# Performance work log

Hardware: AMD Instinct MI355X
Metric: run time of the kernel (lower is better)

Reference implementation:

```python
import jax, jax.numpy as jnp
import numpy as np

B, N, M = 2, 2048, 128
H, D = 16, 64
IN_DIM, CTX_DIM = 1024, 768


def layernorm(x, g, b, eps=1e-5):
    mu = x.mean(-1, keepdims=True)
    var = ((x - mu) ** 2).mean(-1, keepdims=True)
    return (x - mu) * jax.lax.rsqrt(var + eps) * g + b


def setup_inputs() -> dict:
    key = jax.random.key(0)
    ks = jax.random.split(key, 8)
    w = lambda i, sh: jax.random.normal(ks[i], sh, jnp.float32) * 0.02
    return {
        "x": jax.random.normal(ks[0], (B, N, IN_DIM), jnp.float32),
        "c_emb": jax.random.normal(ks[1], (B, M, CTX_DIM), jnp.float32),
        "ln_g": jnp.ones((IN_DIM,), jnp.float32),
        "ln_b": jnp.zeros((IN_DIM,), jnp.float32),
        "ctx_ln_g": jnp.ones((CTX_DIM,), jnp.float32),
        "ctx_ln_b": jnp.zeros((CTX_DIM,), jnp.float32),
        "W_ctx": w(2, (CTX_DIM, 2 * D)),
        "b_ctx": jnp.zeros((2 * D,), jnp.float32),
        "W_q": w(3, (IN_DIM, H * D)),
        "W_kv": w(4, (IN_DIM, 2 * H * D)),
        "null_kv": jax.random.normal(ks[5], (2, D), jnp.float32),
        "W_out": w(6, (H * D, IN_DIM)),
        "out_ln_g": jnp.ones((IN_DIM,), jnp.float32),
        "out_ln_b": jnp.zeros((IN_DIM,), jnp.float32),
    }


def reference(x, c_emb, ln_g, ln_b, ctx_ln_g, ctx_ln_b, W_ctx, b_ctx,
              W_q, W_kv, null_kv, W_out, out_ln_g, out_ln_b):
    b, n, _ = x.shape
    xn = layernorm(x, ln_g, ln_b)
    q = (xn @ W_q).reshape(b, n, H, D)                      # [b,n,h,d]
    kv = (xn @ W_kv).reshape(b, n, 2, H, D)
    k, v = kv[:, :, 0], kv[:, :, 1]                         # [b,n,h,d]
    # context projected to a single shared-across-heads k and v
    ckv = layernorm(c_emb, ctx_ln_g, ctx_ln_b) @ W_ctx + b_ctx
    ck, cv = jnp.split(ckv, 2, axis=-1)                     # [b,m,d]
    nk = jnp.broadcast_to(null_kv[0], (b, 1, D))
    nv = jnp.broadcast_to(null_kv[1], (b, 1, D))
    k_ext = jnp.concatenate([nk, ck], axis=1)               # [b,m+1,d]
    v_ext = jnp.concatenate([nv, cv], axis=1)
    scale = D ** -0.5
    s_self = jnp.einsum('bnhd,bkhd->bhnk', q, k) * scale    # [b,h,n,n]
    s_ctx = jnp.einsum('bnhd,bkd->bhnk', q, k_ext) * scale  # [b,h,n,m+1]
    w = jax.nn.softmax(jnp.concatenate([s_self, s_ctx], axis=-1), axis=-1)
    w_self, w_ctx = w[..., :n], w[..., n:]
    out = (jnp.einsum('bhnk,bkhd->bnhd', w_self, v)
           + jnp.einsum('bhnk,bkd->bnhd', w_ctx, v_ext))    # [b,n,h,d]
    out = out.reshape(b, n, H * D) @ W_out                  # [b,n,input_dim]
    return layernorm(out, out_ln_g, out_ln_b)
```

## Files before the change

### kernel.cpp

```cpp
#include <hip/hip_runtime.h>
#include <cstdint>
#include <cstddef>

typedef __attribute__((ext_vector_type(8))) short bf16x8;
typedef __attribute__((ext_vector_type(4))) short bf16x4;
typedef __attribute__((ext_vector_type(4))) float f32x4;
typedef __attribute__((ext_vector_type(4))) unsigned int u32x4;
typedef __attribute__((ext_vector_type(2))) unsigned int u32x2;

__device__ inline unsigned short f2b(float f){
  unsigned int u = __float_as_uint(f);
  u += 0x7fffu + ((u >> 16) & 1u);
  return (unsigned short)(u >> 16);
}
__device__ inline unsigned int pk2(float a, float b){
  unsigned int ua = __float_as_uint(a) + 0x8000u;
  unsigned int ub = __float_as_uint(b) + 0x8000u;
  return __builtin_amdgcn_perm(ub, ua, 0x07060302u);
}
__device__ inline void gl2lds16(const void* g, void* l){
  __builtin_amdgcn_global_load_lds(
      (const __attribute__((address_space(1))) unsigned int*)g,
      (__attribute__((address_space(3))) unsigned int*)l, 16, 0, 0);
}

#define QSCALE 0.18033688011112042f

__global__ __launch_bounds__(256) void prologue_kernel(
    const float* __restrict__ Wq, const float* __restrict__ Wkv,
    const float* __restrict__ Wout,
    unsigned short* __restrict__ Wqkv_t, unsigned short* __restrict__ Wout_t,
    const float* __restrict__ X, const float* __restrict__ G,
    const float* __restrict__ Bb, unsigned short* __restrict__ xn,
    const float* __restrict__ Cemb, const float* __restrict__ cG,
    const float* __restrict__ cBb, const float* __restrict__ Wctx,
    const float* __restrict__ bctx, const float* __restrict__ nullkv,
    unsigned short* __restrict__ kext, unsigned short* __restrict__ vext_t)
{
  __shared__ __align__(16) char fsm[9216];
  int bid = blockIdx.x;
  int t = threadIdx.x;

  if (bid < 1024){
    short* tile = (short*)fsm;
    int cg0 = (bid & 63) * 64;
    int kt  = (bid >> 6) * 64;
    const float* src; int ld; int col0; unsigned short* dst; int drow0;
    if (cg0 < 1024)      { src = Wq;   ld = 1024; col0 = cg0;        dst = Wqkv_t; drow0 = cg0; }
    else if (cg0 < 3072) { src = Wkv;  ld = 2048; col0 = cg0 - 1024; dst = Wqkv_t; drow0 = cg0; }
    else                 { src = Wout; ld = 1024; col0 = cg0 - 3072; dst = Wout_t; drow0 = cg0 - 3072; }
    #pragma unroll
    for (int i = 0; i < 16; ++i){
      int lin = t + 256*i;
      int k = lin >> 6, c = lin & 63;
      tile[k*72 + c] = (short)f2b(src[(size_t)(kt + k)*ld + col0 + c]);
    }
    __syncthreads();
    #pragma unroll
    for (int i = 0; i < 16; ++i){
      int lin = t + 256*i;
      int c = lin >> 6, k = lin & 63;
      dst[(size_t)(drow0 + c)*1024 + kt + k] = (unsigned short)tile[k*72 + c];
    }
  } else if (bid < 5120){
    int row = bid - 1024;
    float* red = (float*)fsm;
    float4 x = ((const float4*)(X + (size_t)row*1024))[t];
    float s  = x.x + x.y + x.z + x.w;
    float s2 = x.x*x.x + x.y*x.y + x.z*x.z + x.w*x.w;
    #pragma unroll
    for (int o = 32; o > 0; o >>= 1){ s += __shfl_down(s, o); s2 += __shfl_down(s2, o); }
    int w = t >> 6;
    if ((t & 63) == 0){ red[w] = s; red[4 + w] = s2; }
    __syncthreads();
    float mu  = (red[0]+red[1]+red[2]+red[3]) * (1.0f/1024.0f);
    float var = (red[4]+red[5]+red[6]+red[7]) * (1.0f/1024.0f) - mu*mu;
    float rstd = rsqrtf(var + 1e-5f);
    float4 g = ((const float4*)G)[t];
    float4 b = ((const float4*)Bb)[t];
    ushort4 u;
    u.x = f2b((x.x-mu)*rstd*g.x + b.x);
    u.y = f2b((x.y-mu)*rstd*g.y + b.y);
    u.z = f2b((x.z-mu)*rstd*g.z + b.z);
    u.w = f2b((x.w-mu)*rstd*g.w + b.w);
    ((ushort4*)xn)[(size_t)row*256 + t] = u;
  } else {
    int row = bid - 5120;
    int b = row >> 7, m = row & 127;
    bool act = t < 128;
    float* red  = (float*)fsm;
    float* xns  = (float*)(fsm + 16);
    if (act && row < 128){
      int b2 = row >> 6, fr = row & 63;
      int frow = (fr == 0) ? 0 : (128 + fr);
      if (t < 64){
        kext[((size_t)b2*192 + frow)*64 + t] = (frow == 0) ? f2b(nullkv[t]) : (unsigned short)0;
      } else {
        int d = t - 64;
        vext_t[((size_t)b2*64 + d)*192 + frow] = (frow == 0) ? f2b(nullkv[64 + d]) : (unsigned short)0;
      }
    }
    const float* xr = Cemb + (size_t)row*768;
    float v[6]; float s = 0.f, s2 = 0.f;
    if (act){
      #pragma unroll
      for (int j = 0; j < 6; ++j){ float xv = xr[t + 128*j]; v[j] = xv; s += xv; s2 += xv*xv; }
      #pragma unroll
      for (int o = 32; o > 0; o >>= 1){ s += __shfl_down(s, o); s2 += __shfl_down(s2, o); }
      int w = t >> 6;
      if ((t & 63) == 0){ red[w] = s; red[2 + w] = s2; }
    }
    __syncthreads();
    if (act){
      float mu  = (red[0]+red[1]) * (1.0f/768.0f);
      float var = (red[2]+red[3]) * (1.0f/768.0f) - mu*mu;
      float rstd = rsqrtf(var + 1e-5f);
      #pragma unroll
      for (int j = 0; j < 6; ++j){ int c = t + 128*j; xns[c] = (v[j]-mu)*rstd*cG[c] + cBb[c]; }
    }
    __syncthreads();
    if (act){
      float acc = bctx[t];
      #pragma unroll 8
      for (int j = 0; j < 768; ++j) acc += xns[j] * Wctx[j*128 + t];
      unsigned short hv = f2b(acc);
      if (t < 64) kext[((size_t)b*192 + 1 + m)*64 + t] = hv;
      else        vext_t[((size_t)b*64 + (t - 64))*192 + 1 + m] = hv;
    }
  }
}

__global__ __launch_bounds__(256) void ln1024f_kernel(
    const float* __restrict__ X, const float* __restrict__ G,
    const float* __restrict__ Bb, float* __restrict__ out)
{
  int row = blockIdx.x, t = threadIdx.x;
  float4 x = ((const float4*)(X + (size_t)row*1024))[t];
  float s  = x.x + x.y + x.z + x.w;
  float s2 = x.x*x.x + x.y*x.y + x.z*x.z + x.w*x.w;
  #pragma unroll
  for (int o = 32; o > 0; o >>= 1){ s += __shfl_down(s, o); s2 += __shfl_down(s2, o); }
  __shared__ float red[8];
  int w = t >> 6;
  if ((t & 63) == 0){ red[w] = s; red[4 + w] = s2; }
  __syncthreads();
  float mu  = (red[0]+red[1]+red[2]+red[3]) * (1.0f/1024.0f);
  float var = (red[4]+red[5]+red[6]+red[7]) * (1.0f/1024.0f) - mu*mu;
  float rstd = rsqrtf(var + 1e-5f);
  float4 g = ((const float4*)G)[t];
  float4 b = ((const float4*)Bb)[t];
  float4 y;
  y.x = (x.x-mu)*rstd*g.x + b.x;
  y.y = (x.y-mu)*rstd*g.y + b.y;
  y.z = (x.z-mu)*rstd*g.z + b.z;
  y.w = (x.w-mu)*rstd*g.w + b.w;
  ((float4*)out)[(size_t)row*256 + t] = y;
}

#define GEMM_MAINLOOP(A_, Bt_, tM_, tN_)                                        \
  __shared__ __align__(16) short sA[128*64];                                    \
  __shared__ __align__(16) short sB[128*64];                                    \
  int t = threadIdx.x, w = t >> 6, lane = t & 63;                               \
  int wm = w & 1, wn = w >> 1, lm = lane & 15, q = lane >> 4;                   \
  int grow = lane >> 3;                                                         \
  int gchk = ((lane & 7) ^ grow) << 3;                                          \
  f32x4 acc[4][4] = {};                                                         \
  const unsigned short* Aw = A_ + (size_t)(tM_ + w*32 + grow)*1024 + gchk;      \
  const unsigned short* Bw = Bt_ + (size_t)(tN_ + w*32 + grow)*1024 + gchk;     \
  for (int kk = 0; kk < 1024; kk += 64){                                        \
    __syncthreads();                                                            \
    gl2lds16(Aw + kk,            &sA[(w*32     )*64]);                          \
    gl2lds16(Aw + kk +  8*1024,  &sA[(w*32 +  8)*64]);                          \
    gl2lds16(Aw + kk + 16*1024,  &sA[(w*32 + 16)*64]);                          \
    gl2lds16(Aw + kk + 24*1024,  &sA[(w*32 + 24)*64]);                          \
    gl2lds16(Bw + kk,            &sB[(w*32     )*64]);                          \
    gl2lds16(Bw + kk +  8*1024,  &sB[(w*32 +  8)*64]);                          \
    gl2lds16(Bw + kk + 16*1024,  &sB[(w*32 + 16)*64]);                          \
    gl2lds16(Bw + kk + 24*1024,  &sB[(w*32 + 24)*64]);                          \
    __syncthreads();                                                            \
    bf16x8 af[4][2], bfr[4][2];                                                 \
    _Pragma("unroll")                                                           \
    for (int i = 0; i < 4; ++i){                                                \
      int ra = wm*64 + i*16 + lm, rb = wn*64 + i*16 + lm;                       \
      _Pragma("unroll")                                                         \
      for (int hh = 0; hh < 2; ++hh){                                           \
        int sw = ((hh*4 + q) ^ (lm & 7)) << 3;                                  \
        af[i][hh]  = *(const bf16x8*)(&sA[ra*64 + sw]);                         \
        bfr[i][hh] = *(const bf16x8*)(&sB[rb*64 + sw]);                         \
      }                                                                         \
    }                                                                           \
    _Pragma("unroll")                                                           \
    for (int hh = 0; hh < 2; ++hh)                                              \
      _Pragma("unroll")                                                         \
      for (int i = 0; i < 4; ++i)                                               \
        _Pragma("unroll")                                                       \
        for (int j = 0; j < 4; ++j)                                             \
          acc[i][j] = __builtin_amdgcn_mfma_f32_16x16x32_bf16(af[i][hh], bfr[j][hh], acc[i][j], 0, 0, 0); \
  }

__global__ __launch_bounds__(256) void gemm_qkv_kernel(
    const unsigned short* __restrict__ A, const unsigned short* __restrict__ Bt,
    unsigned short* __restrict__ Qb, unsigned short* __restrict__ Kb,
    unsigned short* __restrict__ VtG)
{
  int id = blockIdx.x;
  int xcd = id & 7, r = id >> 3;
  int tM = ((xcd >> 1)*8 + (r & 7)) * 128;
  int tN = ((xcd & 1)*12 + (r >> 3)) * 128;
  GEMM_MAINLOOP(A, Bt, tM, tN)
  if (tN < 1024){
    #pragma unroll
    for (int i = 0; i < 4; ++i){
      int R0 = tM + wm*64 + i*16 + q*4;
      int b = R0 >> 11, n = R0 & 2047;
      #pragma unroll
      for (int j = 0; j < 4; ++j){
        int Cg = tN + wn*64 + j*16 + lm;
        int h = Cg >> 6, d = Cg & 63;
        size_t base = ((((size_t)(b*16 + h) << 11) | n) << 6) + d;
        #pragma unroll
        for (int rr = 0; rr < 4; ++rr)
          Qb[base + (size_t)rr*64] = f2b(acc[i][j][rr] * QSCALE);
      }
    }
  } else if (tN < 2048){
    #pragma unroll
    for (int i = 0; i < 4; ++i){
      int R0 = tM + wm*64 + i*16 + q*4;
      int b = R0 >> 11, n = R0 & 2047;
      #pragma unroll
      for (int j = 0; j < 4; ++j){
        int c2 = tN - 1024 + wn*64 + j*16 + lm;
        int h = c2 >> 6, d = c2 & 63;
        size_t base = ((((size_t)(b*16 + h) << 11) | n) << 6) + d;
        #pragma unroll
        for (int rr = 0; rr < 4; ++rr)
          Kb[base + (size_t)rr*64] = f2b(acc[i][j][rr]);
      }
    }
  } else {
    #pragma unroll
    for (int i = 0; i < 4; ++i){
      int R0 = tM + wm*64 + i*16 + q*4;
      int b = R0 >> 11, n = R0 & 2047;
      #pragma unroll
      for (int j = 0; j < 4; ++j){
        int c2 = tN - 2048 + wn*64 + j*16 + lm;
        int h = c2 >> 6, d = c2 & 63;
        ushort4 u;
        u.x = f2b(acc[i][j][0]); u.y = f2b(acc[i][j][1]);
        u.z = f2b(acc[i][j][2]); u.w = f2b(acc[i][j][3]);
        *(ushort4*)(VtG + ((size_t)(b*16 + h)*64 + d)*2048 + n) = u;
      }
    }
  }
}

__global__ __launch_bounds__(256) void gemm_out_kernel(
    const unsigned short* __restrict__ A, const unsigned short* __restrict__ Bt,
    float* __restrict__ C)
{
  int id = blockIdx.x;
  int xcd = id & 7, r = id >> 3;
  int tM = ((r & 3)*8 + xcd) * 128;
  int tN = (r >> 2) * 128;
  GEMM_MAINLOOP(A, Bt, tM, tN)
  #pragma unroll
  for (int i = 0; i < 4; ++i){
    int R0 = tM + wm*64 + i*16 + q*4;
    #pragma unroll
    for (int j = 0; j < 4; ++j){
      int Cg = tN + wn*64 + j*16 + lm;
      #pragma unroll
      for (int rr = 0; rr < 4; ++rr)
        C[(size_t)(R0 + rr)*1024 + Cg] = acc[i][j][rr];
    }
  }
}

__global__ __launch_bounds__(256, 2) void attn_kernel(
    const unsigned short* __restrict__ Qb, const unsigned short* __restrict__ Kb,
    const unsigned short* __restrict__ VtG, const unsigned short* __restrict__ kext,
    const unsigned short* __restrict__ vext_t, unsigned short* __restrict__ Ob)
{
  __shared__ __align__(16) char smem[54272];
  int id = blockIdx.x;
  int xcd = id & 7, slot = id >> 3;
  int bh = xcd*4 + (slot >> 4);
  int qt = slot & 15;
  int b = bh >> 4, h = bh & 15;
  int t = threadIdx.x, w = t >> 6, lane = t & 63;
  int p = w >> 1, lw = w & 1;
  int lm = lane & 15, q = lane >> 4;

  short* myK = (short*)(smem + p*9216);
  short* myV = (short*)(smem + 18432 + p*9216);
  short* pw  = (short*)(smem + 36864 + w*4352);

  const unsigned short* Qbase = Qb + ((size_t)bh*2048 + qt*128 + lw*64)*64;
  bf16x8 qf[4][2];
  #pragma unroll
  for (int qq = 0; qq < 4; ++qq){
    qf[qq][0] = *(const bf16x8*)(Qbase + (size_t)(qq*16 + lm)*64 + q*8);
    qf[qq][1] = *(const bf16x8*)(Qbase + (size_t)(qq*16 + lm)*64 + q*8 + 32);
  }

  f32x4 o[4][4] = {};
  float l_i[4] = {0.f, 0.f, 0.f, 0.f};

  int pt = t & 127;
  int r0 = pt >> 1, c0 = (pt & 1) << 5;
  const int t0 = p ? 18 : 0;
  const int t1 = p ? 35 : 18;

  u32x4 kr[4], vr[4];
  {
    const unsigned short* kp = Kb + ((size_t)bh*2048 + t0*64 + r0)*64 + c0;
    const unsigned short* vp = VtG + ((size_t)bh*64 + r0)*2048 + t0*64 + c0;
    #pragma unroll
    for (int jj = 0; jj < 4; ++jj){
      kr[jj] = *(const u32x4*)(kp + 8*jj);
      vr[jj] = *(const u32x4*)(vp + 8*jj);
    }
  }

  for (int it = 0; it < 18; ++it){
    int tile = t0 + it;
    bool valid = tile < t1;
    __syncthreads();
    if (valid){
      #pragma unroll
      for (int jj = 0; jj < 4; ++jj){
        *(u32x4*)(&myK[r0*72 + c0 + 8*jj]) = kr[jj];
        *(u32x4*)(&myV[r0*72 + c0 + 8*jj]) = vr[jj];
      }
    }
    __syncthreads();

    int nt = tile + 1;
    if (nt < t1){
      bool ext = nt >= 32;
      int kb = ext ? (nt - 32)*64 : nt*64;
      const unsigned short* kp = ext ? (kext + ((size_t)b*192 + kb + r0)*64 + c0)
                                     : (Kb + ((size_t)bh*2048 + kb + r0)*64 + c0);
      const unsigned short* vp = ext ? (vext_t + ((size_t)b*64 + r0)*192 + kb + c0)
                                     : (VtG + ((size_t)bh*64 + r0)*2048 + kb + c0);
      #pragma unroll
      for (int jj = 0; jj < 4; ++jj){
        kr[jj] = *(const u32x4*)(kp + 8*jj);
        vr[jj] = *(const u32x4*)(vp + 8*jj);
      }
    }
    if (!valid) continue;

    bf16x8 kf[4][2];
    #pragma unroll
    for (int st = 0; st < 4; ++st){
      kf[st][0] = *(const bf16x8*)(&myK[(st*16 + lm)*72 + q*8]);
      kf[st][1] = *(const bf16x8*)(&myK[(st*16 + lm)*72 + q*8 + 32]);
    }

    #pragma unroll
    for (int qp = 0; qp < 2; ++qp){
      f32x4 s[2][4];
      #pragma unroll
      for (int qh = 0; qh < 2; ++qh){
        int qq = qp*2 + qh;
        #pragma unroll
        for (int st = 0; st < 4; ++st){
          f32x4 z = {};
          z = __builtin_amdgcn_mfma_f32_16x16x32_bf16(kf[st][0], qf[qq][0], z, 0, 0, 0);
          s[qh][st] = __builtin_amdgcn_mfma_f32_16x16x32_bf16(kf[st][1], qf[qq][1], z, 0, 0, 0);
        }
      }
      if (tile == 34){
        #pragma unroll
        for (int qh = 0; qh < 2; ++qh)
          #pragma unroll
          for (int st = 0; st < 4; ++st)
            #pragma unroll
            for (int rr = 0; rr < 4; ++rr){
              int key = 128 + st*16 + q*4 + rr;
              if (key >= 129) s[qh][st][rr] = -1e30f;
            }
      }
      #pragma unroll
      for (int qh = 0; qh < 2; ++qh){
        float sm = 0.f;
        #pragma unroll
        for (int st = 0; st < 4; ++st)
          #pragma unroll
          for (int rr = 0; rr < 4; ++rr){
            float pv = __builtin_amdgcn_exp2f(s[qh][st][rr]);
            s[qh][st][rr] = pv; sm += pv;
          }
        l_i[qp*2 + qh] += sm;
        #pragma unroll
        for (int st = 0; st < 4; ++st){
          u32x2 pkd;
          pkd[0] = pk2(s[qh][st][0], s[qh][st][1]);
          pkd[1] = pk2(s[qh][st][2], s[qh][st][3]);
          *(u32x2*)(&pw[(qh*16 + lm)*68 + st*16 + q*4]) = pkd;
        }
      }
      bf16x8 pb[2][2];
      #pragma unroll
      for (int qh = 0; qh < 2; ++qh){
        bf16x4 a0 = *(const bf16x4*)(&pw[(qh*16 + lm)*68 + q*8]);
        bf16x4 a1 = *(const bf16x4*)(&pw[(qh*16 + lm)*68 + q*8 + 4]);
        bf16x4 a2 = *(const bf16x4*)(&pw[(qh*16 + lm)*68 + 32 + q*8]);
        bf16x4 a3 = *(const bf16x4*)(&pw[(qh*16 + lm)*68 + 32 + q*8 + 4]);
        pb[qh][0] = __builtin_shufflevector(a0, a1, 0,1,2,3,4,5,6,7);
        pb[qh][1] = __builtin_shufflevector(a2, a3, 0,1,2,3,4,5,6,7);
      }
      #pragma unroll
      for (int ds = 0; ds < 4; ++ds){
        bf16x8 af0 = *(const bf16x8*)(&myV[(ds*16 + lm)*72 + q*8]);
        bf16x8 af1 = *(const bf16x8*)(&myV[(ds*16 + lm)*72 + q*8 + 32]);
        #pragma unroll
        for (int qh = 0; qh < 2; ++qh){
          int qq = qp*2 + qh;
          o[ds][qq] = __builtin_amdgcn_mfma_f32_16x16x32_bf16(af0, pb[qh][0], o[ds][qq], 0, 0, 0);
          o[ds][qq] = __builtin_amdgcn_mfma_f32_16x16x32_bf16(af1, pb[qh][1], o[ds][qq], 0, 0, 0);
        }
      }
    }
  }

  float* mb = (float*)smem;
  float* reg = mb + lw*4352 + lane*68;
  __syncthreads();
  if (p == 1){
    #pragma unroll
    for (int ds = 0; ds < 4; ++ds)
      #pragma unroll
      for (int qq = 0; qq < 4; ++qq)
        *(f32x4*)(reg + (ds*4 + qq)*4) = o[ds][qq];
    #pragma unroll
    for (int qq = 0; qq < 4; ++qq) reg[64 + qq] = l_i[qq];
  }
  __syncthreads();
  if (p == 0){
    #pragma unroll
    for (int qq = 0; qq < 4; ++qq){
      #pragma unroll
      for (int ds = 0; ds < 4; ++ds){
        f32x4 ov = *(const f32x4*)(reg + (ds*4 + qq)*4);
        o[ds][qq] += ov;
      }
      float l = l_i[qq] + reg[64 + qq];
      l += __shfl_xor(l, 16);
      l += __shfl_xor(l, 32);
      float inv = 1.0f / l;
      int n = qt*128 + lw*64 + qq*16 + lm;
      size_t base = ((size_t)b*2048 + n)*1024 + h*64 + q*4;
      #pragma unroll
      for (int ds = 0; ds < 4; ++ds){
        ushort4 u;
        u.x = f2b(o[ds][qq][0] * inv); u.y = f2b(o[ds][qq][1] * inv);
        u.z = f2b(o[ds][qq][2] * inv); u.w = f2b(o[ds][qq][3] * inv);
        *(ushort4*)(Ob + base + ds*16) = u;
      }
    }
  }
}

extern "C" void kernel_launch(void* const* d_in, const int* in_sizes, int n_in,
                              void* d_out, int out_size, void* d_ws, size_t ws_size,
                              hipStream_t stream)
{
  const float* x       = (const float*)d_in[0];
  const float* c_emb   = (const float*)d_in[1];
  const float* ln_g    = (const float*)d_in[2];
  const float* ln_b    = (const float*)d_in[3];
  const float* ctx_g   = (const float*)d_in[4];
  const float* ctx_b   = (const float*)d_in[5];
  const float* W_ctx   = (const float*)d_in[6];
  const float* b_ctx   = (const float*)d_in[7];
  const float* W_q     = (const float*)d_in[8];
  const float* W_kv    = (const float*)d_in[9];
  const float* null_kv = (const float*)d_in[10];
  const float* W_out   = (const float*)d_in[11];
  const float* oln_g   = (const float*)d_in[12];
  const float* oln_b   = (const float*)d_in[13];
  float* out = (float*)d_out;

  char* p = (char*)d_ws;
  unsigned short* xn     = (unsigned short*)p; p += (size_t)4096*1024*2;
  unsigned short* Wqkv_t = (unsigned short*)p; p += (size_t)3072*1024*2;
  unsigned short* Wout_t = (unsigned short*)p; p += (size_t)1024*1024*2;
  unsigned short* Qb     = (unsigned short*)p; p += (size_t)32*2048*64*2;
  unsigned short* Kb     = (unsigned short*)p; p += (size_t)32*2048*64*2;
  unsigned short* VtG    = (unsigned short*)p; p += (size_t)32*64*2048*2;
  unsigned short* kext   = (unsigned short*)p; p += (size_t)2*192*64*2;
  unsigned short* vext_t = (unsigned short*)p; p += (size_t)2*64*192*2;
  unsigned short* aout   = (unsigned short*)p; p += (size_t)4096*1024*2;
  float*          ptmp   = (float*)p;          p += (size_t)4096*1024*4;

  prologue_kernel<<<5376, 256, 0, stream>>>(
      W_q, W_kv, W_out, Wqkv_t, Wout_t,
      x, ln_g, ln_b, xn,
      c_emb, ctx_g, ctx_b, W_ctx, b_ctx, null_kv, kext, vext_t);
  gemm_qkv_kernel<<<768, 256, 0, stream>>>(xn, Wqkv_t, Qb, Kb, VtG);
  attn_kernel<<<512, 256, 0, stream>>>(Qb, Kb, VtG, kext, vext_t, aout);
  gemm_out_kernel<<<256, 256, 0, stream>>>(aout, Wout_t, ptmp);
  ln1024f_kernel<<<4096, 256, 0, stream>>>(ptmp, oln_g, oln_b, out);
}
```

Baseline: 266.7 us.

## Split-K the output GEMM and halve attention query tile to double grid size

The output projection GEMM now splits K into two halves across twice as many blocks and writes two partial fp32 results. The second partial goes into the Q/K buffer, which is no longer needed at that point, and the final layernorm sums the two partials. The attention kernel now handles 64 queries per block instead of 128 and launches 1024 blocks. Both changes aim to raise occupancy across the CUs, which were underfilled with 256/512 blocks. The cost is extra partial-sum traffic and more redundant K/V loads per query in attention.

```diff
diff --git a/kernel.cpp b/kernel.cpp
--- a/kernel.cpp
+++ b/kernel.cpp
@@ -131,11 +131,15 @@
 }
 
 __global__ __launch_bounds__(256) void ln1024f_kernel(
-    const float* __restrict__ X, const float* __restrict__ G,
-    const float* __restrict__ Bb, float* __restrict__ out)
+    const float* __restrict__ P0, const float* __restrict__ P1,
+    const float* __restrict__ G, const float* __restrict__ Bb,
+    float* __restrict__ out)
 {
   int row = blockIdx.x, t = threadIdx.x;
-  float4 x = ((const float4*)(X + (size_t)row*1024))[t];
+  float4 xa = ((const float4*)(P0 + (size_t)row*1024))[t];
+  float4 xb = ((const float4*)(P1 + (size_t)row*1024))[t];
+  float4 x;
+  x.x = xa.x + xb.x; x.y = xa.y + xb.y; x.z = xa.z + xb.z; x.w = xa.w + xb.w;
   float s  = x.x + x.y + x.z + x.w;
   float s2 = x.x*x.x + x.y*x.y + x.z*x.z + x.w*x.w;
   #pragma unroll
@@ -157,7 +161,7 @@
   ((float4*)out)[(size_t)row*256 + t] = y;
 }
 
-#define GEMM_MAINLOOP(A_, Bt_, tM_, tN_)                                        \
+#define GEMM_MAINLOOP_K(A_, Bt_, tM_, tN_, KLO_, KHI_)                          \
   __shared__ __align__(16) short sA[128*64];                                    \
   __shared__ __align__(16) short sB[128*64];                                    \
   int t = threadIdx.x, w = t >> 6, lane = t & 63;                               \
@@ -167,7 +171,7 @@
   f32x4 acc[4][4] = {};                                                         \
   const unsigned short* Aw = A_ + (size_t)(tM_ + w*32 + grow)*1024 + gchk;      \
   const unsigned short* Bw = Bt_ + (size_t)(tN_ + w*32 + grow)*1024 + gchk;     \
-  for (int kk = 0; kk < 1024; kk += 64){                                        \
+  for (int kk = (KLO_); kk < (KHI_); kk += 64){                                 \
     __syncthreads();                                                            \
     gl2lds16(Aw + kk,            &sA[(w*32     )*64]);                          \
     gl2lds16(Aw + kk +  8*1024,  &sA[(w*32 +  8)*64]);                          \
@@ -198,6 +202,8 @@
           acc[i][j] = __builtin_amdgcn_mfma_f32_16x16x32_bf16(af[i][hh], bfr[j][hh], acc[i][j], 0, 0, 0); \
   }
 
+#define GEMM_MAINLOOP(A_, Bt_, tM_, tN_) GEMM_MAINLOOP_K(A_, Bt_, tM_, tN_, 0, 1024)
+
 __global__ __launch_bounds__(256) void gemm_qkv_kernel(
     const unsigned short* __restrict__ A, const unsigned short* __restrict__ Bt,
     unsigned short* __restrict__ Qb, unsigned short* __restrict__ Kb,
@@ -258,13 +264,16 @@
 
 __global__ __launch_bounds__(256) void gemm_out_kernel(
     const unsigned short* __restrict__ A, const unsigned short* __restrict__ Bt,
-    float* __restrict__ C)
+    float* __restrict__ C0, float* __restrict__ C1)
 {
   int id = blockIdx.x;
   int xcd = id & 7, r = id >> 3;
-  int tM = ((r & 3)*8 + xcd) * 128;
-  int tN = (r >> 2) * 128;
-  GEMM_MAINLOOP(A, Bt, tM, tN)
+  int ks = r & 1;
+  int r2 = r >> 1;
+  int tM = ((r2 & 3)*8 + xcd) * 128;
+  int tN = (r2 >> 2) * 128;
+  float* C = ks ? C1 : C0;
+  GEMM_MAINLOOP_K(A, Bt, tM, tN, ks*512, ks*512 + 512)
   #pragma unroll
   for (int i = 0; i < 4; ++i){
     int R0 = tM + wm*64 + i*16 + q*4;
@@ -286,8 +295,8 @@
   __shared__ __align__(16) char smem[54272];
   int id = blockIdx.x;
   int xcd = id & 7, slot = id >> 3;
-  int bh = xcd*4 + (slot >> 4);
-  int qt = slot & 15;
+  int bh = xcd*4 + (slot >> 5);
+  int q64 = slot & 31;
   int b = bh >> 4, h = bh & 15;
   int t = threadIdx.x, w = t >> 6, lane = t & 63;
   int p = w >> 1, lw = w & 1;
@@ -297,16 +306,16 @@
   short* myV = (short*)(smem + 18432 + p*9216);
   short* pw  = (short*)(smem + 36864 + w*4352);
 
-  const unsigned short* Qbase = Qb + ((size_t)bh*2048 + qt*128 + lw*64)*64;
-  bf16x8 qf[4][2];
+  const unsigned short* Qbase = Qb + ((size_t)bh*2048 + q64*64 + lw*32)*64;
+  bf16x8 qf[2][2];
   #pragma unroll
-  for (int qq = 0; qq < 4; ++qq){
+  for (int qq = 0; qq < 2; ++qq){
     qf[qq][0] = *(const bf16x8*)(Qbase + (size_t)(qq*16 + lm)*64 + q*8);
     qf[qq][1] = *(const bf16x8*)(Qbase + (size_t)(qq*16 + lm)*64 + q*8 + 32);
   }
 
-  f32x4 o[4][4] = {};
-  float l_i[4] = {0.f, 0.f, 0.f, 0.f};
+  f32x4 o[4][2] = {};
+  float l_i[2] = {0.f, 0.f};
 
   int pt = t & 127;
   int r0 = pt >> 1, c0 = (pt & 1) << 5;
@@ -360,99 +369,94 @@
       kf[st][1] = *(const bf16x8*)(&myK[(st*16 + lm)*72 + q*8 + 32]);
     }
 
-    #pragma unroll
-    for (int qp = 0; qp < 2; ++qp){
-      f32x4 s[2][4];
-      #pragma unroll
-      for (int qh = 0; qh < 2; ++qh){
-        int qq = qp*2 + qh;
-        #pragma unroll
-        for (int st = 0; st < 4; ++st){
-          f32x4 z = {};
-          z = __builtin_amdgcn_mfma_f32_16x16x32_bf16(kf[st][0], qf[qq][0], z, 0, 0, 0);
-          s[qh][st] = __builtin_amdgcn_mfma_f32_16x16x32_bf16(kf[st][1], qf[qq][1], z, 0, 0, 0);
-        }
-      }
-      if (tile == 34){
-        #pragma unroll
-        for (int qh = 0; qh < 2; ++qh)
-          #pragma unroll
-          for (int st = 0; st < 4; ++st)
-            #pragma unroll
-            for (int rr = 0; rr < 4; ++rr){
-              int key = 128 + st*16 + q*4 + rr;
-              if (key >= 129) s[qh][st][rr] = -1e30f;
-            }
-      }
-      #pragma unroll
-      for (int qh = 0; qh < 2; ++qh){
-        float sm = 0.f;
+    f32x4 s[2][4];
+    #pragma unroll
+    for (int qh = 0; qh < 2; ++qh){
+      #pragma unroll
+      for (int st = 0; st < 4; ++st){
+        f32x4 z = {};
+        z = __builtin_amdgcn_mfma_f32_16x16x32_bf16(kf[st][0], qf[qh][0], z, 0, 0, 0);
+        s[qh][st] = __builtin_amdgcn_mfma_f32_16x16x32_bf16(kf[st][1], qf[qh][1], z, 0, 0, 0);
+      }
+    }
+    if (tile == 34){
+      #pragma unroll
+      for (int qh = 0; qh < 2; ++qh)
         #pragma unroll
         for (int st = 0; st < 4; ++st)
           #pragma unroll
           for (int rr = 0; rr < 4; ++rr){
-            float pv = __builtin_amdgcn_exp2f(s[qh][st][rr]);
-            s[qh][st][rr] = pv; sm += pv;
+            int key = 128 + st*16 + q*4 + rr;
+            if (key >= 129) s[qh][st][rr] = -1e30f;
           }
-        l_i[qp*2 + qh] += sm;
+    }
+    #pragma unroll
+    for (int qh = 0; qh < 2; ++qh){
+      float sm = 0.f;
+      #pragma unroll
+      for (int st = 0; st < 4; ++st)
         #pragma unroll
-        for (int st = 0; st < 4; ++st){
-          u32x2 pkd;
-          pkd[0] = pk2(s[qh][st][0], s[qh][st][1]);
-          pkd[1] = pk2(s[qh][st][2], s[qh][st][3]);
-          *(u32x2*)(&pw[(qh*16 + lm)*68 + st*16 + q*4]) = pkd;
+        for (int rr = 0; rr < 4; ++rr){
+          float pv = __builtin_amdgcn_exp2f(s[qh][st][rr]);
+          s[qh][st][rr] = pv; sm += pv;
         }
-      }
-      bf16x8 pb[2][2];
+      l_i[qh] += sm;
+      #pragma unroll
+      for (int st = 0; st < 4; ++st){
+        u32x2 pkd;
+        pkd[0] = pk2(s[qh][st][0], s[qh][st][1]);
+        pkd[1] = pk2(s[qh][st][2], s[qh][st][3]);
+        *(u32x2*)(&pw[(qh*16 + lm)*68 + st*16 + q*4]) = pkd;
+      }
+    }
+    bf16x8 pb[2][2];
+    #pragma unroll
+    for (int qh = 0; qh < 2; ++qh){
+      bf16x4 a0 = *(const bf16x4*)(&pw[(qh*16 + lm)*68 + q*8]);
+      bf16x4 a1 = *(const bf16x4*)(&pw[(qh*16 + lm)*68 + q*8 + 4]);
+      bf16x4 a2 = *(const bf16x4*)(&pw[(qh*16 + lm)*68 + 32 + q*8]);
+      bf16x4 a3 = *(const bf16x4*)(&pw[(qh*16 + lm)*68 + 32 + q*8 + 4]);
+      pb[qh][0] = __builtin_shufflevector(a0, a1, 0,1,2,3,4,5,6,7);
+      pb[qh][1] = __builtin_shufflevector(a2, a3, 0,1,2,3,4,5,6,7);
+    }
+    #pragma unroll
+    for (int ds = 0; ds < 4; ++ds){
+      bf16x8 af0 = *(const bf16x8*)(&myV[(ds*16 + lm)*72 + q*8]);
+      bf16x8 af1 = *(const bf16x8*)(&myV[(ds*16 + lm)*72 + q*8 + 32]);
       #pragma unroll
       for (int qh = 0; qh < 2; ++qh){
-        bf16x4 a0 = *(const bf16x4*)(&pw[(qh*16 + lm)*68 + q*8]);
-        bf16x4 a1 = *(const bf16x4*)(&pw[(qh*16 + lm)*68 + q*8 + 4]);
-        bf16x4 a2 = *(const bf16x4*)(&pw[(qh*16 + lm)*68 + 32 + q*8]);
-        bf16x4 a3 = *(const bf16x4*)(&pw[(qh*16 + lm)*68 + 32 + q*8 + 4]);
-        pb[qh][0] = __builtin_shufflevector(a0, a1, 0,1,2,3,4,5,6,7);
-        pb[qh][1] = __builtin_shufflevector(a2, a3, 0,1,2,3,4,5,6,7);
-      }
-      #pragma unroll
-      for (int ds = 0; ds < 4; ++ds){
-        bf16x8 af0 = *(const bf16x8*)(&myV[(ds*16 + lm)*72 + q*8]);
-        bf16x8 af1 = *(const bf16x8*)(&myV[(ds*16 + lm)*72 + q*8 + 32]);
-        #pragma unroll
-        for (int qh = 0; qh < 2; ++qh){
-          int qq = qp*2 + qh;
-          o[ds][qq] = __builtin_amdgcn_mfma_f32_16x16x32_bf16(af0, pb[qh][0], o[ds][qq], 0, 0, 0);
-          o[ds][qq] = __builtin_amdgcn_mfma_f32_16x16x32_bf16(af1, pb[qh][1], o[ds][qq], 0, 0, 0);
-        }
+        o[ds][qh] = __builtin_amdgcn_mfma_f32_16x16x32_bf16(af0, pb[qh][0], o[ds][qh], 0, 0, 0);
+        o[ds][qh] = __builtin_amdgcn_mfma_f32_16x16x32_bf16(af1, pb[qh][1], o[ds][qh], 0, 0, 0);
       }
     }
   }
 
   float* mb = (float*)smem;
-  float* reg = mb + lw*4352 + lane*68;
+  float* reg = mb + lw*2304 + lane*36;
   __syncthreads();
   if (p == 1){
     #pragma unroll
     for (int ds = 0; ds < 4; ++ds)
       #pragma unroll
-      for (int qq = 0; qq < 4; ++qq)
-        *(f32x4*)(reg + (ds*4 + qq)*4) = o[ds][qq];
-    #pragma unroll
-    for (int qq = 0; qq < 4; ++qq) reg[64 + qq] = l_i[qq];
+      for (int qq = 0; qq < 2; ++qq)
+        *(f32x4*)(reg + (ds*2 + qq)*4) = o[ds][qq];
+    #pragma unroll
+    for (int qq = 0; qq < 2; ++qq) reg[32 + qq] = l_i[qq];
   }
   __syncthreads();
   if (p == 0){
     #pragma unroll
-    for (int qq = 0; qq < 4; ++qq){
+    for (int qq = 0; qq < 2; ++qq){
       #pragma unroll
       for (int ds = 0; ds < 4; ++ds){
-        f32x4 ov = *(const f32x4*)(reg + (ds*4 + qq)*4);
+        f32x4 ov = *(const f32x4*)(reg + (ds*2 + qq)*4);
         o[ds][qq] += ov;
       }
-      float l = l_i[qq] + reg[64 + qq];
+      float l = l_i[qq] + reg[32 + qq];
       l += __shfl_xor(l, 16);
       l += __shfl_xor(l, 32);
       float inv = 1.0f / l;
-      int n = qt*128 + lw*64 + qq*16 + lm;
+      int n = q64*64 + lw*32 + qq*16 + lm;
       size_t base = ((size_t)b*2048 + n)*1024 + h*64 + q*4;
       #pragma unroll
       for (int ds = 0; ds < 4; ++ds){
@@ -496,13 +500,14 @@
   unsigned short* vext_t = (unsigned short*)p; p += (size_t)2*64*192*2;
   unsigned short* aout   = (unsigned short*)p; p += (size_t)4096*1024*2;
   float*          ptmp   = (float*)p;          p += (size_t)4096*1024*4;
+  float*          ptmp1  = (float*)Qb;
 
   prologue_kernel<<<5376, 256, 0, stream>>>(
       W_q, W_kv, W_out, Wqkv_t, Wout_t,
       x, ln_g, ln_b, xn,
       c_emb, ctx_g, ctx_b, W_ctx, b_ctx, null_kv, kext, vext_t);
   gemm_qkv_kernel<<<768, 256, 0, stream>>>(xn, Wqkv_t, Qb, Kb, VtG);
-  attn_kernel<<<512, 256, 0, stream>>>(Qb, Kb, VtG, kext, vext_t, aout);
-  gemm_out_kernel<<<256, 256, 0, stream>>>(aout, Wout_t, ptmp);
-  ln1024f_kernel<<<4096, 256, 0, stream>>>(ptmp, oln_g, oln_b, out);
-}
+  attn_kernel<<<1024, 256, 0, stream>>>(Qb, Kb, VtG, kext, vext_t, aout);
+  gemm_out_kernel<<<512, 256, 0, stream>>>(aout, Wout_t, ptmp, ptmp1);
+  ln1024f_kernel<<<4096, 256, 0, stream>>>(ptmp, ptmp1, oln_g, oln_b, out);
+}
```

Measured after the change: 270.6 us. About the same (+1.5%).

## Split-K the output GEMM and swizzle attention LDS tiles

Applied to the files above, without the earlier changes.

The output projection GEMM now runs as a two-way split-K over 512 blocks instead of 256, writing two fp32 partial buffers (the second reuses the Q buffer after attention finishes). The final layernorm kernel sums the two partials before normalizing. This is meant to fill more of the GPU's compute units, at the cost of extra fp32 write and read traffic. Separately, the attention kernel drops its padded K/V/P shared-memory rows in favour of XOR-swizzled unpadded layouts, which shrinks LDS use and could raise occupancy while still avoiding bank conflicts.

```diff
diff --git a/kernel.cpp b/kernel.cpp
--- a/kernel.cpp
+++ b/kernel.cpp
@@ -131,11 +131,15 @@
 }
 
 __global__ __launch_bounds__(256) void ln1024f_kernel(
-    const float* __restrict__ X, const float* __restrict__ G,
-    const float* __restrict__ Bb, float* __restrict__ out)
+    const float* __restrict__ P0, const float* __restrict__ P1,
+    const float* __restrict__ G, const float* __restrict__ Bb,
+    float* __restrict__ out)
 {
   int row = blockIdx.x, t = threadIdx.x;
-  float4 x = ((const float4*)(X + (size_t)row*1024))[t];
+  float4 xa = ((const float4*)(P0 + (size_t)row*1024))[t];
+  float4 xb = ((const float4*)(P1 + (size_t)row*1024))[t];
+  float4 x;
+  x.x = xa.x + xb.x; x.y = xa.y + xb.y; x.z = xa.z + xb.z; x.w = xa.w + xb.w;
   float s  = x.x + x.y + x.z + x.w;
   float s2 = x.x*x.x + x.y*x.y + x.z*x.z + x.w*x.w;
   #pragma unroll
@@ -157,7 +161,7 @@
   ((float4*)out)[(size_t)row*256 + t] = y;
 }
 
-#define GEMM_MAINLOOP(A_, Bt_, tM_, tN_)                                        \
+#define GEMM_MAINLOOP_K(A_, Bt_, tM_, tN_, KLO_, KHI_)                          \
   __shared__ __align__(16) short sA[128*64];                                    \
   __shared__ __align__(16) short sB[128*64];                                    \
   int t = threadIdx.x, w = t >> 6, lane = t & 63;                               \
@@ -167,7 +171,7 @@
   f32x4 acc[4][4] = {};                                                         \
   const unsigned short* Aw = A_ + (size_t)(tM_ + w*32 + grow)*1024 + gchk;      \
   const unsigned short* Bw = Bt_ + (size_t)(tN_ + w*32 + grow)*1024 + gchk;     \
-  for (int kk = 0; kk < 1024; kk += 64){                                        \
+  for (int kk = (KLO_); kk < (KHI_); kk += 64){                                 \
     __syncthreads();                                                            \
     gl2lds16(Aw + kk,            &sA[(w*32     )*64]);                          \
     gl2lds16(Aw + kk +  8*1024,  &sA[(w*32 +  8)*64]);                          \
@@ -198,6 +202,8 @@
           acc[i][j] = __builtin_amdgcn_mfma_f32_16x16x32_bf16(af[i][hh], bfr[j][hh], acc[i][j], 0, 0, 0); \
   }
 
+#define GEMM_MAINLOOP(A_, Bt_, tM_, tN_) GEMM_MAINLOOP_K(A_, Bt_, tM_, tN_, 0, 1024)
+
 __global__ __launch_bounds__(256) void gemm_qkv_kernel(
     const unsigned short* __restrict__ A, const unsigned short* __restrict__ Bt,
     unsigned short* __restrict__ Qb, unsigned short* __restrict__ Kb,
@@ -258,13 +264,16 @@
 
 __global__ __launch_bounds__(256) void gemm_out_kernel(
     const unsigned short* __restrict__ A, const unsigned short* __restrict__ Bt,
-    float* __restrict__ C)
+    float* __restrict__ C0, float* __restrict__ C1)
 {
   int id = blockIdx.x;
   int xcd = id & 7, r = id >> 3;
-  int tM = ((r & 3)*8 + xcd) * 128;
-  int tN = (r >> 2) * 128;
-  GEMM_MAINLOOP(A, Bt, tM, tN)
+  int ks = r & 1;
+  int r2 = r >> 1;
+  int tM = ((r2 & 3)*8 + xcd) * 128;
+  int tN = (r2 >> 2) * 128;
+  float* C = ks ? C1 : C0;
+  GEMM_MAINLOOP_K(A, Bt, tM, tN, ks*512, ks*512 + 512)
   #pragma unroll
   for (int i = 0; i < 4; ++i){
     int R0 = tM + wm*64 + i*16 + q*4;
@@ -283,7 +292,7 @@
     const unsigned short* __restrict__ VtG, const unsigned short* __restrict__ kext,
     const unsigned short* __restrict__ vext_t, unsigned short* __restrict__ Ob)
 {
-  __shared__ __align__(16) char smem[54272];
+  __shared__ __align__(16) char smem[40960];
   int id = blockIdx.x;
   int xcd = id & 7, slot = id >> 3;
   int bh = xcd*4 + (slot >> 4);
@@ -292,10 +301,11 @@
   int t = threadIdx.x, w = t >> 6, lane = t & 63;
   int p = w >> 1, lw = w & 1;
   int lm = lane & 15, q = lane >> 4;
-
-  short* myK = (short*)(smem + p*9216);
-  short* myV = (short*)(smem + 18432 + p*9216);
-  short* pw  = (short*)(smem + 36864 + w*4352);
+  int esw = lm & 7;
+
+  short* myK = (short*)(smem + p*8192);
+  short* myV = (short*)(smem + 16384 + p*8192);
+  short* pw  = (short*)(smem + 32768 + w*2048);
 
   const unsigned short* Qbase = Qb + ((size_t)bh*2048 + qt*128 + lw*64)*64;
   bf16x8 qf[4][2];
@@ -310,6 +320,7 @@
 
   int pt = t & 127;
   int r0 = pt >> 1, c0 = (pt & 1) << 5;
+  int rsw = r0 & 7;
   const int t0 = p ? 18 : 0;
   const int t1 = p ? 35 : 18;
 
@@ -331,8 +342,9 @@
     if (valid){
       #pragma unroll
       for (int jj = 0; jj < 4; ++jj){
-        *(u32x4*)(&myK[r0*72 + c0 + 8*jj]) = kr[jj];
-        *(u32x4*)(&myV[r0*72 + c0 + 8*jj]) = vr[jj];
+        int gsw = ((((pt & 1) << 2) | jj) ^ rsw) << 3;
+        *(u32x4*)(&myK[r0*64 + gsw]) = kr[jj];
+        *(u32x4*)(&myV[r0*64 + gsw]) = vr[jj];
       }
     }
     __syncthreads();
@@ -356,8 +368,8 @@
     bf16x8 kf[4][2];
     #pragma unroll
     for (int st = 0; st < 4; ++st){
-      kf[st][0] = *(const bf16x8*)(&myK[(st*16 + lm)*72 + q*8]);
-      kf[st][1] = *(const bf16x8*)(&myK[(st*16 + lm)*72 + q*8 + 32]);
+      kf[st][0] = *(const bf16x8*)(&myK[(st*16 + lm)*64 + ((q       ^ esw) << 3)]);
+      kf[st][1] = *(const bf16x8*)(&myK[(st*16 + lm)*64 + (((4 + q) ^ esw) << 3)]);
     }
 
     #pragma unroll
@@ -384,6 +396,7 @@
               if (key >= 129) s[qh][st][rr] = -1e30f;
             }
       }
+      bf16x8 pb[2][2];
       #pragma unroll
       for (int qh = 0; qh < 2; ++qh){
         float sm = 0.f;
@@ -400,23 +413,20 @@
           u32x2 pkd;
           pkd[0] = pk2(s[qh][st][0], s[qh][st][1]);
           pkd[1] = pk2(s[qh][st][2], s[qh][st][3]);
-          *(u32x2*)(&pw[(qh*16 + lm)*68 + st*16 + q*4]) = pkd;
+          int gsw = ((((st << 1) | (q >> 1)) ^ esw) << 3) + ((q & 1) << 2);
+          *(u32x2*)(&pw[lm*64 + gsw]) = pkd;
         }
-      }
-      bf16x8 pb[2][2];
-      #pragma unroll
-      for (int qh = 0; qh < 2; ++qh){
-        bf16x4 a0 = *(const bf16x4*)(&pw[(qh*16 + lm)*68 + q*8]);
-        bf16x4 a1 = *(const bf16x4*)(&pw[(qh*16 + lm)*68 + q*8 + 4]);
-        bf16x4 a2 = *(const bf16x4*)(&pw[(qh*16 + lm)*68 + 32 + q*8]);
-        bf16x4 a3 = *(const bf16x4*)(&pw[(qh*16 + lm)*68 + 32 + q*8 + 4]);
+        bf16x4 a0 = *(const bf16x4*)(&pw[lm*64 + ((q       ^ esw) << 3)]);
+        bf16x4 a1 = *(const bf16x4*)(&pw[lm*64 + ((q       ^ esw) << 3) + 4]);
+        bf16x4 a2 = *(const bf16x4*)(&pw[lm*64 + (((4 + q) ^ esw) << 3)]);
+        bf16x4 a3 = *(const bf16x4*)(&pw[lm*64 + (((4 + q) ^ esw) << 3) + 4]);
         pb[qh][0] = __builtin_shufflevector(a0, a1, 0,1,2,3,4,5,6,7);
         pb[qh][1] = __builtin_shufflevector(a2, a3, 0,1,2,3,4,5,6,7);
       }
       #pragma unroll
       for (int ds = 0; ds < 4; ++ds){
-        bf16x8 af0 = *(const bf16x8*)(&myV[(ds*16 + lm)*72 + q*8]);
-        bf16x8 af1 = *(const bf16x8*)(&myV[(ds*16 + lm)*72 + q*8 + 32]);
+        bf16x8 af0 = *(const bf16x8*)(&myV[(ds*16 + lm)*64 + ((q       ^ esw) << 3)]);
+        bf16x8 af1 = *(const bf16x8*)(&myV[(ds*16 + lm)*64 + (((4 + q) ^ esw) << 3)]);
         #pragma unroll
         for (int qh = 0; qh < 2; ++qh){
           int qq = qp*2 + qh;
@@ -496,6 +506,7 @@
   unsigned short* vext_t = (unsigned short*)p; p += (size_t)2*64*192*2;
   unsigned short* aout   = (unsigned short*)p; p += (size_t)4096*1024*2;
   float*          ptmp   = (float*)p;          p += (size_t)4096*1024*4;
+  float*          ptmp1  = (float*)Qb;
 
   prologue_kernel<<<5376, 256, 0, stream>>>(
       W_q, W_kv, W_out, Wqkv_t, Wout_t,
@@ -503,6 +514,6 @@
       c_emb, ctx_g, ctx_b, W_ctx, b_ctx, null_kv, kext, vext_t);
   gemm_qkv_kernel<<<768, 256, 0, stream>>>(xn, Wqkv_t, Qb, Kb, VtG);
   attn_kernel<<<512, 256, 0, stream>>>(Qb, Kb, VtG, kext, vext_t, aout);
-  gemm_out_kernel<<<256, 256, 0, stream>>>(aout, Wout_t, ptmp);
-  ln1024f_kernel<<<4096, 256, 0, stream>>>(ptmp, oln_g, oln_b, out);
-}
+  gemm_out_kernel<<<512, 256, 0, stream>>>(aout, Wout_t, ptmp, ptmp1);
+  ln1024f_kernel<<<4096, 256, 0, stream>>>(ptmp, ptmp1, oln_g, oln_b, out);
+}
```

Measured after the change: 259.5 us. -2.7%, faster.
